# Performance work log

Measured on AMD Instinct MI355X. Metric: run time of the kernel, lower is better.

Reference implementation:

```python
import jax, jax.numpy as jnp
import numpy as np

K = 4                 # max_block_size (depthwise conv kernel size)
BLOCKS = (1, 2, 3, 4) # block sizes, offset 0
DS = 4                # downsample_factor
BLOCK_MULT = 12       # lcm(1,2,3,4)
DIM = 512
NUM_TOKENS = 256


def setup_inputs() -> dict:
    key = jax.random.key(0)
    ks = jax.random.split(key, 8)
    b, n = 4, 4096
    s = 0.02
    return {
        "x": jax.random.randint(ks[0], (b, n), 0, NUM_TOKENS),
        "emb": jax.random.normal(ks[1], (NUM_TOKENS, DIM), dtype=jnp.float32) * s,
        "conv_w": jax.random.normal(ks[2], (DIM, K), dtype=jnp.float32) * s,   # depthwise Conv1d weight [d,1,K] squeezed
        "conv_b": jax.random.normal(ks[3], (DIM,), dtype=jnp.float32) * s,
        "proj_w": jax.random.normal(ks[4], (DIM, DIM), dtype=jnp.float32) * s,  # 1x1 conv == linear [out,in]
        "proj_b": jax.random.normal(ks[5], (DIM,), dtype=jnp.float32) * s,
        "score_w": jax.random.normal(ks[6], (DIM,), dtype=jnp.float32) * s,     # nn.Linear(dim,1)
        "score_b": jax.random.normal(ks[7], (), dtype=jnp.float32) * s,
    }


def reference(x, emb, conv_w, conv_b, proj_w, proj_b, score_w, score_b):
    b, n = x.shape
    h = emb[x]  # [b, n, d] token embedding (gather)

    # pos_conv: pad (K-1) at sequence end, depthwise conv (valid), then pointwise proj
    hp = jnp.pad(h, ((0, 0), (0, K - 1), (0, 0)))
    y = conv_b + sum(hp[:, k:k + n, :] * conv_w[:, k] for k in range(K))  # [b, n, d]
    h = y @ proj_w.T + proj_b

    # pad sequence to multiple of lcm of block sizes
    L = -(-n // BLOCK_MULT) * BLOCK_MULT
    h = jnp.pad(h, ((0, 0), (0, L - n), (0, 0)))

    # multi-scale block mean pooling, upsampled back to length L
    reprs = []
    for bs in BLOCKS:
        r = h.reshape(b, L // bs, bs, DIM).mean(axis=2)     # [b, L/bs, d]
        reprs.append(jnp.repeat(r, bs, axis=1))             # [b, L, d]
    block_reprs = jnp.stack(reprs, axis=2)                  # [b, L, nb, d]

    # per-position block scores
    scores = block_reprs @ score_w + score_b                # [b, L, nb]
    scores = jax.nn.softmax(scores, axis=2)

    # consensus attention over positions (d = nb = len(BLOCKS))
    sim = jnp.einsum('bid,bjd->bij', scores, scores)        # [b, L, L]
    attn = jax.nn.softmax(sim, axis=-1)
    scores = jnp.einsum('bij,bjm->bim', attn, scores)       # [b, L, nb]

    # fuse block representations and downsample
    out = jnp.einsum('bnkd,bnk->bnd', block_reprs, scores)  # [b, L, d]
    m = -(-n // DS) * DS                                    # == n (4096 divisible by 4)
    out = out[:, :m].reshape(b, m // DS, DS, DIM).mean(axis=2)
    return out
```

## Files before the change

kernel.cpp:

```cpp
#include <hip/hip_runtime.h>
#include <hip/hip_bf16.h>

#define B_ 4
#define N_ 4096
#define L_ 4104
#define D_ 512
#define BK 64
#define NF 210
#define ZCH 36
#define ZCHUNKS 114
#define PST 37

typedef __attribute__((ext_vector_type(8))) short bf16x8;
typedef __attribute__((ext_vector_type(4))) float f32x4;

__global__ __launch_bounds__(256) void k_g(const float* __restrict__ emb,
    const float* __restrict__ pw, const float* __restrict__ cwp,
    const float* __restrict__ cb, const float* __restrict__ pb,
    float* __restrict__ G, float* __restrict__ biasp,
    unsigned* __restrict__ featPk, float* __restrict__ featCf,
    float* __restrict__ Zg) {
  __shared__ __align__(16) __hip_bfloat16 As[2][64 * BK];
  __shared__ __align__(16) __hip_bfloat16 Bs[2][128 * BK];
  __shared__ __align__(16) float cwS[512];
  __shared__ float red[4];
  const int bx = blockIdx.x;
  const int t = threadIdx.x;
  const int w = t >> 6, l = t & 63;

  if (bx == 128) {
    for (int zi = t; zi < B_ * NF * 5; zi += 256) Zg[zi] = 0.f;
    if (t < NF) {
      int idx = 0, mp = 0, mq = 0, mr = 0, ms = 0;
      for (int m = 0; m <= 6; ++m)
        for (int p = m; p >= 0; --p)
          for (int q = m - p; q >= 0; --q)
            for (int r = m - p - q; r >= 0; --r) {
              const int s4 = m - p - q - r;
              if (idx == t) { mp = p; mq = q; mr = r; ms = s4; }
              ++idx;
            }
      featPk[t] = (unsigned)mp | ((unsigned)mq << 8) | ((unsigned)mr << 16) | ((unsigned)ms << 24);
      const float invf[7] = {1.f, 1.f, 0.5f, 1.f/6.f, 1.f/24.f, 1.f/120.f, 1.f/720.f};
      featCf[t] = invf[mp] * invf[mq] * invf[mr] * invf[ms];
    }
    return;
  }
  if (bx >= 64) {
    const int o0 = (bx - 64) * 8;
    const float2 cv = *(const float2*)(cb + t * 2);
#pragma unroll
    for (int oo = 0; oo < 8; ++oo) {
      const int o = o0 + oo;
      const float2 wv = *(const float2*)(pw + (size_t)o * 512 + t * 2);
      float s = wv.x * cv.x + wv.y * cv.y;
#pragma unroll
      for (int off = 32; off > 0; off >>= 1) s += __shfl_xor(s, off);
      if (l == 0) red[w] = s;
      __syncthreads();
      if (t == 0) biasp[o] = red[0] + red[1] + red[2] + red[3] + pb[o];
      __syncthreads();
    }
    return;
  }

  const int m0 = (bx & 3) * 64;
  const int n0 = ((bx >> 2) & 3) * 128;
  const int kp = bx >> 4;
  const int quad = l >> 4, r16 = l & 15;
  const int wc = w * 32;

  cwS[t]       = cwp[t * 4 + kp];
  cwS[t + 256] = cwp[(t + 256) * 4 + kp];

  f32x4 acc[4][2];
#pragma unroll
  for (int a = 0; a < 4; ++a)
#pragma unroll
    for (int bq = 0; bq < 2; ++bq) acc[a][bq] = (f32x4){0.f, 0.f, 0.f, 0.f};

  const int ra = t >> 2, ga0 = (t & 3) * 2;
  const int rb = t >> 1, gb0 = (t & 1) * 4;

#define STAGEG(buf, kb)                                                          \
  _Pragma("unroll")                                                              \
  for (int gi = 0; gi < 2; ++gi) {                                               \
    const int g = ga0 + gi;                                                      \
    const int c0 = (kb) + g * 8;                                                 \
    const float4 a0 = *(const float4*)(emb + (size_t)(m0 + ra) * 512 + c0);      \
    const float4 a1 = *(const float4*)(emb + (size_t)(m0 + ra) * 512 + c0 + 4);  \
    const float4 w0 = *(const float4*)(cwS + c0);                                \
    const float4 w1 = *(const float4*)(cwS + c0 + 4);                            \
    union { __hip_bfloat16 q[8]; bf16x8 v; } ua;                                 \
    ua.q[0] = __float2bfloat16(a0.x * w0.x); ua.q[1] = __float2bfloat16(a0.y * w0.y); \
    ua.q[2] = __float2bfloat16(a0.z * w0.z); ua.q[3] = __float2bfloat16(a0.w * w0.w); \
    ua.q[4] = __float2bfloat16(a1.x * w1.x); ua.q[5] = __float2bfloat16(a1.y * w1.y); \
    ua.q[6] = __float2bfloat16(a1.z * w1.z); ua.q[7] = __float2bfloat16(a1.w * w1.w); \
    *(bf16x8*)(&As[buf][ra * BK + ((g ^ (ra & 7)) * 8)]) = ua.v;                 \
  }                                                                              \
  _Pragma("unroll")                                                              \
  for (int gi = 0; gi < 4; ++gi) {                                               \
    const int g = gb0 + gi;                                                      \
    const int c0 = (kb) + g * 8;                                                 \
    const float4 b0 = *(const float4*)(pw + (size_t)(n0 + rb) * 512 + c0);       \
    const float4 b1 = *(const float4*)(pw + (size_t)(n0 + rb) * 512 + c0 + 4);   \
    union { __hip_bfloat16 q[8]; bf16x8 v; } ub;                                 \
    ub.q[0] = __float2bfloat16(b0.x); ub.q[1] = __float2bfloat16(b0.y);          \
    ub.q[2] = __float2bfloat16(b0.z); ub.q[3] = __float2bfloat16(b0.w);          \
    ub.q[4] = __float2bfloat16(b1.x); ub.q[5] = __float2bfloat16(b1.y);          \
    ub.q[6] = __float2bfloat16(b1.z); ub.q[7] = __float2bfloat16(b1.w);          \
    *(bf16x8*)(&Bs[buf][rb * BK + ((g ^ (rb & 7)) * 8)]) = ub.v;                 \
  }

  __syncthreads();
  STAGEG(0, 0)
  __syncthreads();

#pragma unroll 1
  for (int kt = 0; kt < 8; ++kt) {
    const int cur = kt & 1;
    if (kt < 7) { STAGEG(1 - cur, (kt + 1) * BK) }
#pragma unroll
    for (int kk = 0; kk < 2; ++kk) {
      const int col_e = (kk * 32 + quad * 8) ^ ((r16 & 7) * 8);
      bf16x8 af[4], bfr[2];
#pragma unroll
      for (int ti = 0; ti < 4; ++ti)
        af[ti] = *(const bf16x8*)(&As[cur][(ti * 16 + r16) * BK + col_e]);
#pragma unroll
      for (int tj = 0; tj < 2; ++tj)
        bfr[tj] = *(const bf16x8*)(&Bs[cur][(wc + tj * 16 + r16) * BK + col_e]);
#pragma unroll
      for (int ti = 0; ti < 4; ++ti)
#pragma unroll
        for (int tj = 0; tj < 2; ++tj)
          acc[ti][tj] = __builtin_amdgcn_mfma_f32_16x16x32_bf16(af[ti], bfr[tj], acc[ti][tj], 0, 0, 0);
    }
    __syncthreads();
  }
#undef STAGEG

#pragma unroll
  for (int ti = 0; ti < 4; ++ti) {
    const int gi0 = m0 + ti * 16 + quad * 4;
#pragma unroll
    for (int tj = 0; tj < 2; ++tj) {
      const int go = n0 + wc + tj * 16 + r16;
#pragma unroll
      for (int r = 0; r < 4; ++r)
        G[((size_t)kp * 256 + gi0 + r) * 512 + go] = acc[ti][tj][r];
    }
  }
}

__global__ __launch_bounds__(256) void k_ts(const float* __restrict__ G,
    const float* __restrict__ biasp, const float* __restrict__ sw,
    float* __restrict__ TS, float* __restrict__ c0g) {
  __shared__ float red[4];
  const int bx = blockIdx.x;
  const int t = threadIdx.x, w = t >> 6, l = t & 63;
  if (bx == 128) {
    const float2 a = *(const float2*)(biasp + t * 2);
    const float2 b = *(const float2*)(sw + t * 2);
    float s = a.x * b.x + a.y * b.y;
#pragma unroll
    for (int off = 32; off > 0; off >>= 1) s += __shfl_xor(s, off);
    if (l == 0) red[w] = s;
    __syncthreads();
    if (t == 0) c0g[0] = red[0] + red[1] + red[2] + red[3];
    return;
  }
  const float4 s0 = *(const float4*)(sw + l * 8);
  const float4 s1 = *(const float4*)(sw + l * 8 + 4);
#pragma unroll
  for (int rr = 0; rr < 2; ++rr) {
    const int row = bx * 8 + w * 2 + rr;
    const float4 g0 = *(const float4*)(G + (size_t)row * 512 + l * 8);
    const float4 g1 = *(const float4*)(G + (size_t)row * 512 + l * 8 + 4);
    float s = g0.x * s0.x + g0.y * s0.y + g0.z * s0.z + g0.w * s0.w
            + g1.x * s1.x + g1.y * s1.y + g1.z * s1.z + g1.w * s1.w;
#pragma unroll
    for (int off = 32; off > 0; off >>= 1) s += __shfl_xor(s, off);
    if (l == 0) TS[row] = s;
  }
}

__device__ __forceinline__ float4 softmax4(const float* __restrict__ tw, int base,
                                           int i, float bb) {
  const float s0 = tw[i - base] + bb;
  const int j2 = i & ~1;
  const float s1 = (tw[j2 - base] + tw[j2 + 1 - base]) * 0.5f + bb;
  const int j3 = (i / 3) * 3;
  const float s2 = (tw[j3 - base] + tw[j3 + 1 - base] + tw[j3 + 2 - base]) * (1.f / 3.f) + bb;
  const int j4 = i & ~3;
  const float s3 = (tw[j4 - base] + tw[j4 + 1 - base] + tw[j4 + 2 - base] + tw[j4 + 3 - base]) * 0.25f + bb;
  const float m = fmaxf(fmaxf(s0, s1), fmaxf(s2, s3));
  const float e0 = __expf(s0 - m), e1 = __expf(s1 - m), e2 = __expf(s2 - m), e3 = __expf(s3 - m);
  const float inv = 1.f / (e0 + e1 + e2 + e3);
  return make_float4(e0 * inv, e1 * inv, e2 * inv, e3 * inv);
}

__global__ __launch_bounds__(256) void k_zphi(const int* __restrict__ x,
    const float* __restrict__ TS, const float* __restrict__ c0g,
    const float* __restrict__ sb, const unsigned* __restrict__ featPk,
    float* __restrict__ Zg) {
  __shared__ float twj[ZCH];
  __shared__ float P[32][PST];
  __shared__ unsigned pkS[NF];
  __shared__ int tokS[ZCH + 3];
  const int bx = blockIdx.x;
  const int b = bx / ZCHUNKS, jc = bx % ZCHUNKS;
  const int t = threadIdx.x;
  const int j0 = jc * ZCH;
  if (t < NF) pkS[t] = featPk[t];
  if (t < ZCH + 3) {
    const int j = j0 + t;
    tokS[t] = (j < N_) ? x[b * N_ + j] : -1;
  }
  __syncthreads();
  if (t < ZCH) {
    float tv = 0.f;
    if (j0 + t < N_) {
      tv = c0g[0];
#pragma unroll
      for (int k = 0; k < 4; ++k) {
        const int tk = tokS[t + k];
        if (tk >= 0) tv += TS[k * 256 + tk];
      }
    }
    twj[t] = tv;
  }
  __syncthreads();
  const float bb = sb[0];
  if (t < ZCH) {
    const float4 s = softmax4(twj, j0, j0 + t, bb);
    P[0][t] = 1.f; P[8][t] = 1.f; P[16][t] = 1.f; P[24][t] = 1.f;
    float va = 1.f, vb = 1.f, vc = 1.f, vd = 1.f;
#pragma unroll
    for (int e = 1; e < 8; ++e) {
      va *= s.x; vb *= s.y; vc *= s.z; vd *= s.w;
      P[e][t] = va; P[8 + e][t] = vb; P[16 + e][t] = vc; P[24 + e][t] = vd;
    }
  }
  __syncthreads();
  if (t < NF) {
    const unsigned pk = pkS[t];
    const int p = pk & 255, q = (pk >> 8) & 255, r = (pk >> 16) & 255, s4 = pk >> 24;
    const float* Ra0 = &P[p][0];       const float* Ra1 = &P[p + 1][0];
    const float* Rb0 = &P[8 + q][0];   const float* Rb1 = &P[8 + q + 1][0];
    const float* Rc0 = &P[16 + r][0];  const float* Rc1 = &P[16 + r + 1][0];
    const float* Rd0 = &P[24 + s4][0]; const float* Rd1 = &P[24 + s4 + 1][0];
    float z0 = 0.f, z1 = 0.f, z2 = 0.f, z3 = 0.f, z4 = 0.f;
#pragma unroll 4
    for (int jj = 0; jj < ZCH; ++jj) {
      const float pa0 = Ra0[jj], pa1 = Ra1[jj];
      const float pb0 = Rb0[jj], pb1 = Rb1[jj];
      const float pc0 = Rc0[jj], pc1 = Rc1[jj];
      const float pd0 = Rd0[jj], pd1 = Rd1[jj];
      const float cd = pc0 * pd0, ab = pa0 * pb0;
      z4 += pa0 * (pb0 * cd);
      z0 += pa1 * (pb0 * cd);
      z1 += pb1 * (pa0 * cd);
      z2 += pc1 * (ab * pd0);
      z3 += pd1 * (ab * pc0);
    }
    float* zb = Zg + (size_t)(b * NF + t) * 5;
    atomicAdd(zb + 0, z0); atomicAdd(zb + 1, z1); atomicAdd(zb + 2, z2);
    atomicAdd(zb + 3, z3); atomicAdd(zb + 4, z4);
  }
}

__global__ __launch_bounds__(256) void k_fuse(const int* __restrict__ x,
    const float* __restrict__ G, const float* __restrict__ biasp,
    const float* __restrict__ TS, const float* __restrict__ c0g,
    const float* __restrict__ sb, const unsigned* __restrict__ featPk,
    const float* __restrict__ featCf, const float* __restrict__ Zg,
    float* __restrict__ out) {
  __shared__ __align__(16) float4 wgtS[12];
  __shared__ float tbS[12];
  __shared__ float Pr[12][33];
  __shared__ float Zl[NF * 5];
  __shared__ unsigned pkS[NF];
  __shared__ float cfS[NF];
  __shared__ int tokS[16];
  const int bx = blockIdx.x;
  const int b = bx / 342, j12 = bx % 342;
  const int t = threadIdx.x, d = t * 2;
  const int r0 = 12 * j12;

  if (t < NF) { pkS[t] = featPk[t]; cfS[t] = featCf[t]; }
  for (int i2 = t; i2 < NF * 5; i2 += 256) Zl[i2] = Zg[(size_t)b * NF * 5 + i2];
  if (t < 15) {
    const int j = r0 + t;
    tokS[t] = (j < N_) ? x[b * N_ + j] : -1;
  }
  __syncthreads();

  const float2 bp = *(const float2*)(biasp + d);
  float2 hv[12];
#pragma unroll
  for (int q = 0; q < 12; ++q) {
    float2 a = make_float2(0.f, 0.f);
    if (r0 + q < N_) {
      a = bp;
#pragma unroll
      for (int k = 0; k < 4; ++k) {
        const int tk = tokS[q + k];
        if (tk >= 0) {
          const float2 g = *(const float2*)(G + ((size_t)k * 256 + tk) * 512 + d);
          a.x += g.x; a.y += g.y;
        }
      }
    }
    hv[q] = a;
  }

  if (t < 12) {
    float tv = 0.f;
    if (r0 + t < N_) {
      tv = c0g[0];
#pragma unroll
      for (int k = 0; k < 4; ++k) {
        const int tk = tokS[t + k];
        if (tk >= 0) tv += TS[k * 256 + tk];
      }
    }
    tbS[t] = tv;
  }
  __syncthreads();
  if (t < 12) {
    const float4 s = softmax4(tbS, r0, r0 + t, sb[0]);
    float* p = &Pr[t][0];
    float va = 1.f, vb = 1.f, vc = 1.f, vd = 1.f;
    p[0] = 1.f; p[8] = 1.f; p[16] = 1.f; p[24] = 1.f;
#pragma unroll
    for (int e = 1; e < 8; ++e) {
      va *= s.x; vb *= s.y; vc *= s.z; vd *= s.w;
      p[e] = va; p[8 + e] = vb; p[16 + e] = vc; p[24 + e] = vd;
    }
  }
  __syncthreads();
  if (t < 192) {
    const int row = t >> 4, fi = t & 15;
    float n0 = 0.f, n1 = 0.f, n2 = 0.f, n3 = 0.f, dn = 0.f;
    const float* pr = &Pr[row][0];
    for (int f = fi; f < NF; f += 16) {
      const unsigned pk = pkS[f];
      const float val = cfS[f] * pr[pk & 255] * pr[8 + ((pk >> 8) & 255)]
                                * pr[16 + ((pk >> 16) & 255)] * pr[24 + (pk >> 24)];
      const float* z = &Zl[f * 5];
      n0 += val * z[0]; n1 += val * z[1]; n2 += val * z[2]; n3 += val * z[3];
      dn += val * z[4];
    }
#pragma unroll
    for (int m = 8; m >= 1; m >>= 1) {
      n0 += __shfl_xor(n0, m); n1 += __shfl_xor(n1, m); n2 += __shfl_xor(n2, m);
      n3 += __shfl_xor(n3, m); dn += __shfl_xor(dn, m);
    }
    if (fi == 0) {
      const float inv = 1.f / dn;
      wgtS[row] = make_float4(n0 * inv, n1 * inv, n2 * inv, n3 * inv);
    }
  }
  __syncthreads();

  float2 p2[6], p3[4], p4[3];
#pragma unroll
  for (int g = 0; g < 6; ++g) {
    p2[g].x = (hv[2 * g].x + hv[2 * g + 1].x) * 0.5f;
    p2[g].y = (hv[2 * g].y + hv[2 * g + 1].y) * 0.5f;
  }
#pragma unroll
  for (int g = 0; g < 4; ++g) {
    p3[g].x = (hv[3 * g].x + hv[3 * g + 1].x + hv[3 * g + 2].x) * (1.f / 3.f);
    p3[g].y = (hv[3 * g].y + hv[3 * g + 1].y + hv[3 * g + 2].y) * (1.f / 3.f);
  }
#pragma unroll
  for (int g = 0; g < 3; ++g) {
    p4[g].x = (hv[4 * g].x + hv[4 * g + 1].x + hv[4 * g + 2].x + hv[4 * g + 3].x) * 0.25f;
    p4[g].y = (hv[4 * g].y + hv[4 * g + 1].y + hv[4 * g + 2].y + hv[4 * g + 3].y) * 0.25f;
  }

#pragma unroll
  for (int o = 0; o < 3; ++o) {
    const int orow = j12 * 3 + o;
    if (orow < 1024) {
      float ox = 0.f, oy = 0.f;
#pragma unroll
      for (int rr = 0; rr < 4; ++rr) {
        const int r = 4 * o + rr;
        const float4 wv = wgtS[r];
        const float2 p1 = hv[r];
        const float2 q2 = p2[r >> 1];
        const float2 q3 = p3[r / 3];
        const float2 q4 = p4[o];
        ox += wv.x * p1.x + wv.y * q2.x + wv.z * q3.x + wv.w * q4.x;
        oy += wv.x * p1.y + wv.y * q2.y + wv.z * q3.y + wv.w * q4.y;
      }
      float2 ov; ov.x = ox * 0.25f; ov.y = oy * 0.25f;
      *(float2*)(out + (size_t)(b * 1024 + orow) * D_ + d) = ov;
    }
  }
}

extern "C" void kernel_launch(void* const* d_in, const int* in_sizes, int n_in,
                              void* d_out, int out_size, void* d_ws, size_t ws_size,
                              hipStream_t stream) {
  const int*   x       = (const int*)d_in[0];
  const float* emb     = (const float*)d_in[1];
  const float* conv_w  = (const float*)d_in[2];
  const float* conv_b  = (const float*)d_in[3];
  const float* proj_w  = (const float*)d_in[4];
  const float* proj_b  = (const float*)d_in[5];
  const float* score_w = (const float*)d_in[6];
  const float* score_b = (const float*)d_in[7];
  float* out = (float*)d_out;

  char* ws = (char*)d_ws;
  size_t off = 0;
  float*    G      = (float*)(ws + off); off += (size_t)4 * 256 * 512 * 4;
  float*    bias   = (float*)(ws + off); off += (size_t)512 * 4;
  float*    Zg     = (float*)(ws + off); off += (size_t)B_ * NF * 5 * 4;
  unsigned* featPk = (unsigned*)(ws + off); off += (size_t)1024;
  float*    featCf = (float*)(ws + off); off += (size_t)1024;
  float*    TS     = (float*)(ws + off); off += (size_t)1024 * 4;
  float*    c0     = (float*)(ws + off); off += (size_t)16;
  (void)in_sizes; (void)n_in; (void)out_size; (void)ws_size;

  k_g<<<129, 256, 0, stream>>>(emb, proj_w, conv_w, conv_b, proj_b, G, bias, featPk, featCf, Zg);
  k_ts<<<129, 256, 0, stream>>>(G, bias, score_w, TS, c0);
  k_zphi<<<B_ * ZCHUNKS, 256, 0, stream>>>(x, TS, c0, score_b, featPk, Zg);
  k_fuse<<<B_ * 342, 256, 0, stream>>>(x, G, bias, TS, c0, score_b, featPk, featCf, Zg, out);
}
```

Before: 137.1 us.

## Merge four kernels into one cooperative persistent kernel with grid syncs

Replaces the four separate launches (GEMM, score projection, Z accumulation, fuse) with one cooperative kernel of 512 blocks. Phases are separated by grid.sync, and shared memory is overlaid through a union. The fuse phase now loops over tiles in grid-stride fashion. This removes launch gaps and inter-kernel drain costs, at the price of grid-wide barriers, a fixed grid size and lower per-phase parallelism in the fuse stage.

```diff
diff --git a/kernel.cpp b/kernel.cpp
--- a/kernel.cpp
+++ b/kernel.cpp
@@ -1,5 +1,8 @@
 #include <hip/hip_runtime.h>
 #include <hip/hip_bf16.h>
+#include <hip/hip_cooperative_groups.h>
+
+namespace cg = cooperative_groups;
 
 #define B_ 4
 #define N_ 4096
@@ -10,77 +13,68 @@
 #define ZCH 36
 #define ZCHUNKS 114
 #define PST 37
+#define GRID 512
 
 typedef __attribute__((ext_vector_type(8))) short bf16x8;
 typedef __attribute__((ext_vector_type(4))) float f32x4;
 
-__global__ __launch_bounds__(256) void k_g(const float* __restrict__ emb,
-    const float* __restrict__ pw, const float* __restrict__ cwp,
-    const float* __restrict__ cb, const float* __restrict__ pb,
+struct GS { __hip_bfloat16 As[2][64 * BK]; __hip_bfloat16 Bs[2][128 * BK]; float cwS[512]; };
+struct ZS { float twj[ZCH]; float P[32][PST]; unsigned pkS[NF]; int tokS[ZCH + 3]; };
+struct FS { float wgtS[48]; float tbS[12]; float Pr[12][33]; float Zl[NF * 5];
+            unsigned pkS[NF]; float cfS[NF]; int tokS[16]; };
+
+__device__ __forceinline__ float4 softmax4(const float* __restrict__ tw, int base,
+                                           int i, float bb) {
+  const float s0 = tw[i - base] + bb;
+  const int j2 = i & ~1;
+  const float s1 = (tw[j2 - base] + tw[j2 + 1 - base]) * 0.5f + bb;
+  const int j3 = (i / 3) * 3;
+  const float s2 = (tw[j3 - base] + tw[j3 + 1 - base] + tw[j3 + 2 - base]) * (1.f / 3.f) + bb;
+  const int j4 = i & ~3;
+  const float s3 = (tw[j4 - base] + tw[j4 + 1 - base] + tw[j4 + 2 - base] + tw[j4 + 3 - base]) * 0.25f + bb;
+  const float m = fmaxf(fmaxf(s0, s1), fmaxf(s2, s3));
+  const float e0 = __expf(s0 - m), e1 = __expf(s1 - m), e2 = __expf(s2 - m), e3 = __expf(s3 - m);
+  const float inv = 1.f / (e0 + e1 + e2 + e3);
+  return make_float4(e0 * inv, e1 * inv, e2 * inv, e3 * inv);
+}
+
+__global__ __launch_bounds__(256, 2) void k_all(const int* __restrict__ x,
+    const float* __restrict__ emb, const float* __restrict__ cwp,
+    const float* __restrict__ cb, const float* __restrict__ pw,
+    const float* __restrict__ pb, const float* __restrict__ sw,
+    const float* __restrict__ sb,
     float* __restrict__ G, float* __restrict__ biasp,
     unsigned* __restrict__ featPk, float* __restrict__ featCf,
-    float* __restrict__ Zg) {
-  __shared__ __align__(16) __hip_bfloat16 As[2][64 * BK];
-  __shared__ __align__(16) __hip_bfloat16 Bs[2][128 * BK];
-  __shared__ __align__(16) float cwS[512];
+    float* __restrict__ Zg, float* __restrict__ TS, float* __restrict__ c0g,
+    float* __restrict__ out) {
+  __shared__ __align__(16) union { GS g; ZS z; FS f; } u;
   __shared__ float red[4];
+  cg::grid_group grid = cg::this_grid();
   const int bx = blockIdx.x;
   const int t = threadIdx.x;
-  const int w = t >> 6, l = t & 63;
-
-  if (bx == 128) {
-    for (int zi = t; zi < B_ * NF * 5; zi += 256) Zg[zi] = 0.f;
-    if (t < NF) {
-      int idx = 0, mp = 0, mq = 0, mr = 0, ms = 0;
-      for (int m = 0; m <= 6; ++m)
-        for (int p = m; p >= 0; --p)
-          for (int q = m - p; q >= 0; --q)
-            for (int r = m - p - q; r >= 0; --r) {
-              const int s4 = m - p - q - r;
-              if (idx == t) { mp = p; mq = q; mr = r; ms = s4; }
-              ++idx;
-            }
-      featPk[t] = (unsigned)mp | ((unsigned)mq << 8) | ((unsigned)mr << 16) | ((unsigned)ms << 24);
-      const float invf[7] = {1.f, 1.f, 0.5f, 1.f/6.f, 1.f/24.f, 1.f/120.f, 1.f/720.f};
-      featCf[t] = invf[mp] * invf[mq] * invf[mr] * invf[ms];
-    }
-    return;
-  }
-  if (bx >= 64) {
-    const int o0 = (bx - 64) * 8;
-    const float2 cv = *(const float2*)(cb + t * 2);
-#pragma unroll
-    for (int oo = 0; oo < 8; ++oo) {
-      const int o = o0 + oo;
-      const float2 wv = *(const float2*)(pw + (size_t)o * 512 + t * 2);
-      float s = wv.x * cv.x + wv.y * cv.y;
-#pragma unroll
-      for (int off = 32; off > 0; off >>= 1) s += __shfl_xor(s, off);
-      if (l == 0) red[w] = s;
-      __syncthreads();
-      if (t == 0) biasp[o] = red[0] + red[1] + red[2] + red[3] + pb[o];
-      __syncthreads();
-    }
-    return;
-  }
-
-  const int m0 = (bx & 3) * 64;
-  const int n0 = ((bx >> 2) & 3) * 128;
-  const int kp = bx >> 4;
-  const int quad = l >> 4, r16 = l & 15;
-  const int wc = w * 32;
-
-  cwS[t]       = cwp[t * 4 + kp];
-  cwS[t + 256] = cwp[(t + 256) * 4 + kp];
-
-  f32x4 acc[4][2];
-#pragma unroll
-  for (int a = 0; a < 4; ++a)
-#pragma unroll
-    for (int bq = 0; bq < 2; ++bq) acc[a][bq] = (f32x4){0.f, 0.f, 0.f, 0.f};
-
-  const int ra = t >> 2, ga0 = (t & 3) * 2;
-  const int rb = t >> 1, gb0 = (t & 1) * 4;
+
+  if (bx < 64) {
+    const int w = t >> 6, l = t & 63;
+    const int m0 = (bx & 3) * 64;
+    const int n0 = ((bx >> 2) & 3) * 128;
+    const int kp = bx >> 4;
+    const int quad = l >> 4, r16 = l & 15;
+    const int wc = w * 32;
+    auto& As = u.g.As;
+    auto& Bs = u.g.Bs;
+    float* cwS = u.g.cwS;
+
+    cwS[t]       = cwp[t * 4 + kp];
+    cwS[t + 256] = cwp[(t + 256) * 4 + kp];
+
+    f32x4 acc[4][2];
+#pragma unroll
+    for (int a = 0; a < 4; ++a)
+#pragma unroll
+      for (int bq = 0; bq < 2; ++bq) acc[a][bq] = (f32x4){0.f, 0.f, 0.f, 0.f};
+
+    const int ra = t >> 2, ga0 = (t & 3) * 2;
+    const int rb = t >> 1, gb0 = (t & 1) * 4;
 
 #define STAGEG(buf, kb)                                                          \
   _Pragma("unroll")                                                              \
@@ -112,69 +106,85 @@
     *(bf16x8*)(&Bs[buf][rb * BK + ((g ^ (rb & 7)) * 8)]) = ub.v;                 \
   }
 
-  __syncthreads();
-  STAGEG(0, 0)
-  __syncthreads();
+    __syncthreads();
+    STAGEG(0, 0)
+    __syncthreads();
 
 #pragma unroll 1
-  for (int kt = 0; kt < 8; ++kt) {
-    const int cur = kt & 1;
-    if (kt < 7) { STAGEG(1 - cur, (kt + 1) * BK) }
-#pragma unroll
-    for (int kk = 0; kk < 2; ++kk) {
-      const int col_e = (kk * 32 + quad * 8) ^ ((r16 & 7) * 8);
-      bf16x8 af[4], bfr[2];
-#pragma unroll
-      for (int ti = 0; ti < 4; ++ti)
-        af[ti] = *(const bf16x8*)(&As[cur][(ti * 16 + r16) * BK + col_e]);
-#pragma unroll
-      for (int tj = 0; tj < 2; ++tj)
-        bfr[tj] = *(const bf16x8*)(&Bs[cur][(wc + tj * 16 + r16) * BK + col_e]);
-#pragma unroll
-      for (int ti = 0; ti < 4; ++ti)
+    for (int kt = 0; kt < 8; ++kt) {
+      const int cur = kt & 1;
+      if (kt < 7) { STAGEG(1 - cur, (kt + 1) * BK) }
+#pragma unroll
+      for (int kk = 0; kk < 2; ++kk) {
+        const int col_e = (kk * 32 + quad * 8) ^ ((r16 & 7) * 8);
+        bf16x8 af[4], bfr[2];
+#pragma unroll
+        for (int ti = 0; ti < 4; ++ti)
+          af[ti] = *(const bf16x8*)(&As[cur][(ti * 16 + r16) * BK + col_e]);
 #pragma unroll
         for (int tj = 0; tj < 2; ++tj)
-          acc[ti][tj] = __builtin_amdgcn_mfma_f32_16x16x32_bf16(af[ti], bfr[tj], acc[ti][tj], 0, 0, 0);
-    }
-    __syncthreads();
+          bfr[tj] = *(const bf16x8*)(&Bs[cur][(wc + tj * 16 + r16) * BK + col_e]);
+#pragma unroll
+        for (int ti = 0; ti < 4; ++ti)
+#pragma unroll
+          for (int tj = 0; tj < 2; ++tj)
+            acc[ti][tj] = __builtin_amdgcn_mfma_f32_16x16x32_bf16(af[ti], bfr[tj], acc[ti][tj], 0, 0, 0);
+      }
+      __syncthreads();
+    }
+#undef STAGEG
+
+#pragma unroll
+    for (int ti = 0; ti < 4; ++ti) {
+      const int gi0 = m0 + ti * 16 + quad * 4;
+#pragma unroll
+      for (int tj = 0; tj < 2; ++tj) {
+        const int go = n0 + wc + tj * 16 + r16;
+#pragma unroll
+        for (int r = 0; r < 4; ++r)
+          G[((size_t)kp * 256 + gi0 + r) * 512 + go] = acc[ti][tj][r];
+      }
+    }
+  } else if (bx < 96) {
+    const int w = t >> 6, l = t & 63;
+    const float4 cb0 = *(const float4*)(cb + l * 8);
+    const float4 cb1 = *(const float4*)(cb + l * 8 + 4);
+#pragma unroll
+    for (int i = 0; i < 4; ++i) {
+      const int o = (bx - 64) * 16 + w * 4 + i;
+      const float4 w0 = *(const float4*)(pw + (size_t)o * 512 + l * 8);
+      const float4 w1 = *(const float4*)(pw + (size_t)o * 512 + l * 8 + 4);
+      float s = w0.x * cb0.x + w0.y * cb0.y + w0.z * cb0.z + w0.w * cb0.w
+              + w1.x * cb1.x + w1.y * cb1.y + w1.z * cb1.z + w1.w * cb1.w;
+#pragma unroll
+      for (int off = 32; off > 0; off >>= 1) s += __shfl_xor(s, off);
+      if (l == 0) biasp[o] = s + pb[o];
+    }
+  } else if (bx == 96) {
+    for (int zi = t; zi < B_ * NF * 5; zi += 256) Zg[zi] = 0.f;
+    if (t < NF) {
+      int idx = 0, mp = 0, mq = 0, mr = 0, ms = 0;
+      for (int m = 0; m <= 6; ++m)
+        for (int p = m; p >= 0; --p)
+          for (int q = m - p; q >= 0; --q)
+            for (int r = m - p - q; r >= 0; --r) {
+              const int s4 = m - p - q - r;
+              if (idx == t) { mp = p; mq = q; mr = r; ms = s4; }
+              ++idx;
+            }
+      featPk[t] = (unsigned)mp | ((unsigned)mq << 8) | ((unsigned)mr << 16) | ((unsigned)ms << 24);
+      const float invf[7] = {1.f, 1.f, 0.5f, 1.f/6.f, 1.f/24.f, 1.f/120.f, 1.f/720.f};
+      featCf[t] = invf[mp] * invf[mq] * invf[mr] * invf[ms];
+    }
   }
-#undef STAGEG
-
-#pragma unroll
-  for (int ti = 0; ti < 4; ++ti) {
-    const int gi0 = m0 + ti * 16 + quad * 4;
-#pragma unroll
-    for (int tj = 0; tj < 2; ++tj) {
-      const int go = n0 + wc + tj * 16 + r16;
-#pragma unroll
-      for (int r = 0; r < 4; ++r)
-        G[((size_t)kp * 256 + gi0 + r) * 512 + go] = acc[ti][tj][r];
-    }
-  }
-}
-
-__global__ __launch_bounds__(256) void k_ts(const float* __restrict__ G,
-    const float* __restrict__ biasp, const float* __restrict__ sw,
-    float* __restrict__ TS, float* __restrict__ c0g) {
-  __shared__ float red[4];
-  const int bx = blockIdx.x;
-  const int t = threadIdx.x, w = t >> 6, l = t & 63;
-  if (bx == 128) {
-    const float2 a = *(const float2*)(biasp + t * 2);
-    const float2 b = *(const float2*)(sw + t * 2);
-    float s = a.x * b.x + a.y * b.y;
-#pragma unroll
-    for (int off = 32; off > 0; off >>= 1) s += __shfl_xor(s, off);
-    if (l == 0) red[w] = s;
-    __syncthreads();
-    if (t == 0) c0g[0] = red[0] + red[1] + red[2] + red[3];
-    return;
-  }
-  const float4 s0 = *(const float4*)(sw + l * 8);
-  const float4 s1 = *(const float4*)(sw + l * 8 + 4);
-#pragma unroll
-  for (int rr = 0; rr < 2; ++rr) {
-    const int row = bx * 8 + w * 2 + rr;
+
+  grid.sync();
+
+  if (bx < 256) {
+    const int w = t >> 6, l = t & 63;
+    const int row = bx * 4 + w;
+    const float4 s0 = *(const float4*)(sw + l * 8);
+    const float4 s1 = *(const float4*)(sw + l * 8 + 4);
     const float4 g0 = *(const float4*)(G + (size_t)row * 512 + l * 8);
     const float4 g1 = *(const float4*)(G + (size_t)row * 512 + l * 8 + 4);
     float s = g0.x * s0.x + g0.y * s0.y + g0.z * s0.z + g0.w * s0.w
@@ -182,223 +192,208 @@
 #pragma unroll
     for (int off = 32; off > 0; off >>= 1) s += __shfl_xor(s, off);
     if (l == 0) TS[row] = s;
+  } else if (bx == 256) {
+    const int w = t >> 6, l = t & 63;
+    const float2 a = *(const float2*)(biasp + t * 2);
+    const float2 b = *(const float2*)(sw + t * 2);
+    float s = a.x * b.x + a.y * b.y;
+#pragma unroll
+    for (int off = 32; off > 0; off >>= 1) s += __shfl_xor(s, off);
+    if (l == 0) red[w] = s;
+    __syncthreads();
+    if (t == 0) c0g[0] = red[0] + red[1] + red[2] + red[3];
   }
-}
-
-__device__ __forceinline__ float4 softmax4(const float* __restrict__ tw, int base,
-                                           int i, float bb) {
-  const float s0 = tw[i - base] + bb;
-  const int j2 = i & ~1;
-  const float s1 = (tw[j2 - base] + tw[j2 + 1 - base]) * 0.5f + bb;
-  const int j3 = (i / 3) * 3;
-  const float s2 = (tw[j3 - base] + tw[j3 + 1 - base] + tw[j3 + 2 - base]) * (1.f / 3.f) + bb;
-  const int j4 = i & ~3;
-  const float s3 = (tw[j4 - base] + tw[j4 + 1 - base] + tw[j4 + 2 - base] + tw[j4 + 3 - base]) * 0.25f + bb;
-  const float m = fmaxf(fmaxf(s0, s1), fmaxf(s2, s3));
-  const float e0 = __expf(s0 - m), e1 = __expf(s1 - m), e2 = __expf(s2 - m), e3 = __expf(s3 - m);
-  const float inv = 1.f / (e0 + e1 + e2 + e3);
-  return make_float4(e0 * inv, e1 * inv, e2 * inv, e3 * inv);
-}
-
-__global__ __launch_bounds__(256) void k_zphi(const int* __restrict__ x,
-    const float* __restrict__ TS, const float* __restrict__ c0g,
-    const float* __restrict__ sb, const unsigned* __restrict__ featPk,
-    float* __restrict__ Zg) {
-  __shared__ float twj[ZCH];
-  __shared__ float P[32][PST];
-  __shared__ unsigned pkS[NF];
-  __shared__ int tokS[ZCH + 3];
-  const int bx = blockIdx.x;
-  const int b = bx / ZCHUNKS, jc = bx % ZCHUNKS;
-  const int t = threadIdx.x;
-  const int j0 = jc * ZCH;
-  if (t < NF) pkS[t] = featPk[t];
-  if (t < ZCH + 3) {
-    const int j = j0 + t;
-    tokS[t] = (j < N_) ? x[b * N_ + j] : -1;
+
+  grid.sync();
+
+  if (bx < B_ * ZCHUNKS) {
+    const int b = bx / ZCHUNKS, jc = bx % ZCHUNKS;
+    const int j0 = jc * ZCH;
+    float* twj = u.z.twj;
+    float (&P)[32][PST] = u.z.P;
+    unsigned* pkS = u.z.pkS;
+    int* tokS = u.z.tokS;
+    if (t < NF) pkS[t] = featPk[t];
+    if (t < ZCH + 3) {
+      const int j = j0 + t;
+      tokS[t] = (j < N_) ? x[b * N_ + j] : -1;
+    }
+    __syncthreads();
+    if (t < ZCH) {
+      float tv = 0.f;
+      if (j0 + t < N_) {
+        tv = c0g[0];
+#pragma unroll
+        for (int k = 0; k < 4; ++k) {
+          const int tk = tokS[t + k];
+          if (tk >= 0) tv += TS[k * 256 + tk];
+        }
+      }
+      twj[t] = tv;
+    }
+    __syncthreads();
+    const float bb = sb[0];
+    if (t < ZCH) {
+      const float4 s = softmax4(twj, j0, j0 + t, bb);
+      P[0][t] = 1.f; P[8][t] = 1.f; P[16][t] = 1.f; P[24][t] = 1.f;
+      float va = 1.f, vb = 1.f, vc = 1.f, vd = 1.f;
+#pragma unroll
+      for (int e = 1; e < 8; ++e) {
+        va *= s.x; vb *= s.y; vc *= s.z; vd *= s.w;
+        P[e][t] = va; P[8 + e][t] = vb; P[16 + e][t] = vc; P[24 + e][t] = vd;
+      }
+    }
+    __syncthreads();
+    if (t < NF) {
+      const unsigned pk = pkS[t];
+      const int p = pk & 255, q = (pk >> 8) & 255, r = (pk >> 16) & 255, s4 = pk >> 24;
+      const float* Ra0 = &P[p][0];       const float* Ra1 = &P[p + 1][0];
+      const float* Rb0 = &P[8 + q][0];   const float* Rb1 = &P[8 + q + 1][0];
+      const float* Rc0 = &P[16 + r][0];  const float* Rc1 = &P[16 + r + 1][0];
+      const float* Rd0 = &P[24 + s4][0]; const float* Rd1 = &P[24 + s4 + 1][0];
+      float z0 = 0.f, z1 = 0.f, z2 = 0.f, z3 = 0.f, z4 = 0.f;
+#pragma unroll 4
+      for (int jj = 0; jj < ZCH; ++jj) {
+        const float pa0 = Ra0[jj], pa1 = Ra1[jj];
+        const float pb0 = Rb0[jj], pb1 = Rb1[jj];
+        const float pc0 = Rc0[jj], pc1 = Rc1[jj];
+        const float pd0 = Rd0[jj], pd1 = Rd1[jj];
+        const float cd = pc0 * pd0, ab = pa0 * pb0;
+        z4 += pa0 * (pb0 * cd);
+        z0 += pa1 * (pb0 * cd);
+        z1 += pb1 * (pa0 * cd);
+        z2 += pc1 * (ab * pd0);
+        z3 += pd1 * (ab * pc0);
+      }
+      float* zb = Zg + (size_t)(b * NF + t) * 5;
+      atomicAdd(zb + 0, z0); atomicAdd(zb + 1, z1); atomicAdd(zb + 2, z2);
+      atomicAdd(zb + 3, z3); atomicAdd(zb + 4, z4);
+    }
   }
-  __syncthreads();
-  if (t < ZCH) {
-    float tv = 0.f;
-    if (j0 + t < N_) {
-      tv = c0g[0];
-#pragma unroll
-      for (int k = 0; k < 4; ++k) {
-        const int tk = tokS[t + k];
-        if (tk >= 0) tv += TS[k * 256 + tk];
-      }
-    }
-    twj[t] = tv;
-  }
-  __syncthreads();
-  const float bb = sb[0];
-  if (t < ZCH) {
-    const float4 s = softmax4(twj, j0, j0 + t, bb);
-    P[0][t] = 1.f; P[8][t] = 1.f; P[16][t] = 1.f; P[24][t] = 1.f;
-    float va = 1.f, vb = 1.f, vc = 1.f, vd = 1.f;
-#pragma unroll
-    for (int e = 1; e < 8; ++e) {
-      va *= s.x; vb *= s.y; vc *= s.z; vd *= s.w;
-      P[e][t] = va; P[8 + e][t] = vb; P[16 + e][t] = vc; P[24 + e][t] = vd;
-    }
-  }
-  __syncthreads();
-  if (t < NF) {
-    const unsigned pk = pkS[t];
-    const int p = pk & 255, q = (pk >> 8) & 255, r = (pk >> 16) & 255, s4 = pk >> 24;
-    const float* Ra0 = &P[p][0];       const float* Ra1 = &P[p + 1][0];
-    const float* Rb0 = &P[8 + q][0];   const float* Rb1 = &P[8 + q + 1][0];
-    const float* Rc0 = &P[16 + r][0];  const float* Rc1 = &P[16 + r + 1][0];
-    const float* Rd0 = &P[24 + s4][0]; const float* Rd1 = &P[24 + s4 + 1][0];
-    float z0 = 0.f, z1 = 0.f, z2 = 0.f, z3 = 0.f, z4 = 0.f;
-#pragma unroll 4
-    for (int jj = 0; jj < ZCH; ++jj) {
-      const float pa0 = Ra0[jj], pa1 = Ra1[jj];
-      const float pb0 = Rb0[jj], pb1 = Rb1[jj];
-      const float pc0 = Rc0[jj], pc1 = Rc1[jj];
-      const float pd0 = Rd0[jj], pd1 = Rd1[jj];
-      const float cd = pc0 * pd0, ab = pa0 * pb0;
-      z4 += pa0 * (pb0 * cd);
-      z0 += pa1 * (pb0 * cd);
-      z1 += pb1 * (pa0 * cd);
-      z2 += pc1 * (ab * pd0);
-      z3 += pd1 * (ab * pc0);
-    }
-    float* zb = Zg + (size_t)(b * NF + t) * 5;
-    atomicAdd(zb + 0, z0); atomicAdd(zb + 1, z1); atomicAdd(zb + 2, z2);
-    atomicAdd(zb + 3, z3); atomicAdd(zb + 4, z4);
-  }
-}
-
-__global__ __launch_bounds__(256) void k_fuse(const int* __restrict__ x,
-    const float* __restrict__ G, const float* __restrict__ biasp,
-    const float* __restrict__ TS, const float* __restrict__ c0g,
-    const float* __restrict__ sb, const unsigned* __restrict__ featPk,
-    const float* __restrict__ featCf, const float* __restrict__ Zg,
-    float* __restrict__ out) {
-  __shared__ __align__(16) float4 wgtS[12];
-  __shared__ float tbS[12];
-  __shared__ float Pr[12][33];
-  __shared__ float Zl[NF * 5];
-  __shared__ unsigned pkS[NF];
-  __shared__ float cfS[NF];
-  __shared__ int tokS[16];
-  const int bx = blockIdx.x;
-  const int b = bx / 342, j12 = bx % 342;
-  const int t = threadIdx.x, d = t * 2;
-  const int r0 = 12 * j12;
-
-  if (t < NF) { pkS[t] = featPk[t]; cfS[t] = featCf[t]; }
-  for (int i2 = t; i2 < NF * 5; i2 += 256) Zl[i2] = Zg[(size_t)b * NF * 5 + i2];
-  if (t < 15) {
-    const int j = r0 + t;
-    tokS[t] = (j < N_) ? x[b * N_ + j] : -1;
-  }
-  __syncthreads();
-
-  const float2 bp = *(const float2*)(biasp + d);
-  float2 hv[12];
-#pragma unroll
-  for (int q = 0; q < 12; ++q) {
-    float2 a = make_float2(0.f, 0.f);
-    if (r0 + q < N_) {
-      a = bp;
-#pragma unroll
-      for (int k = 0; k < 4; ++k) {
-        const int tk = tokS[q + k];
-        if (tk >= 0) {
-          const float2 g = *(const float2*)(G + ((size_t)k * 256 + tk) * 512 + d);
-          a.x += g.x; a.y += g.y;
-        }
-      }
-    }
-    hv[q] = a;
-  }
-
-  if (t < 12) {
-    float tv = 0.f;
-    if (r0 + t < N_) {
-      tv = c0g[0];
-#pragma unroll
-      for (int k = 0; k < 4; ++k) {
-        const int tk = tokS[t + k];
-        if (tk >= 0) tv += TS[k * 256 + tk];
-      }
-    }
-    tbS[t] = tv;
-  }
-  __syncthreads();
-  if (t < 12) {
-    const float4 s = softmax4(tbS, r0, r0 + t, sb[0]);
-    float* p = &Pr[t][0];
-    float va = 1.f, vb = 1.f, vc = 1.f, vd = 1.f;
-    p[0] = 1.f; p[8] = 1.f; p[16] = 1.f; p[24] = 1.f;
-#pragma unroll
-    for (int e = 1; e < 8; ++e) {
-      va *= s.x; vb *= s.y; vc *= s.z; vd *= s.w;
-      p[e] = va; p[8 + e] = vb; p[16 + e] = vc; p[24 + e] = vd;
-    }
-  }
-  __syncthreads();
-  if (t < 192) {
-    const int row = t >> 4, fi = t & 15;
-    float n0 = 0.f, n1 = 0.f, n2 = 0.f, n3 = 0.f, dn = 0.f;
-    const float* pr = &Pr[row][0];
-    for (int f = fi; f < NF; f += 16) {
-      const unsigned pk = pkS[f];
-      const float val = cfS[f] * pr[pk & 255] * pr[8 + ((pk >> 8) & 255)]
-                                * pr[16 + ((pk >> 16) & 255)] * pr[24 + (pk >> 24)];
-      const float* z = &Zl[f * 5];
-      n0 += val * z[0]; n1 += val * z[1]; n2 += val * z[2]; n3 += val * z[3];
-      dn += val * z[4];
-    }
-#pragma unroll
-    for (int m = 8; m >= 1; m >>= 1) {
-      n0 += __shfl_xor(n0, m); n1 += __shfl_xor(n1, m); n2 += __shfl_xor(n2, m);
-      n3 += __shfl_xor(n3, m); dn += __shfl_xor(dn, m);
-    }
-    if (fi == 0) {
-      const float inv = 1.f / dn;
-      wgtS[row] = make_float4(n0 * inv, n1 * inv, n2 * inv, n3 * inv);
-    }
-  }
-  __syncthreads();
-
-  float2 p2[6], p3[4], p4[3];
-#pragma unroll
-  for (int g = 0; g < 6; ++g) {
-    p2[g].x = (hv[2 * g].x + hv[2 * g + 1].x) * 0.5f;
-    p2[g].y = (hv[2 * g].y + hv[2 * g + 1].y) * 0.5f;
-  }
-#pragma unroll
-  for (int g = 0; g < 4; ++g) {
-    p3[g].x = (hv[3 * g].x + hv[3 * g + 1].x + hv[3 * g + 2].x) * (1.f / 3.f);
-    p3[g].y = (hv[3 * g].y + hv[3 * g + 1].y + hv[3 * g + 2].y) * (1.f / 3.f);
-  }
-#pragma unroll
-  for (int g = 0; g < 3; ++g) {
-    p4[g].x = (hv[4 * g].x + hv[4 * g + 1].x + hv[4 * g + 2].x + hv[4 * g + 3].x) * 0.25f;
-    p4[g].y = (hv[4 * g].y + hv[4 * g + 1].y + hv[4 * g + 2].y + hv[4 * g + 3].y) * 0.25f;
-  }
-
-#pragma unroll
-  for (int o = 0; o < 3; ++o) {
-    const int orow = j12 * 3 + o;
-    if (orow < 1024) {
-      float ox = 0.f, oy = 0.f;
-#pragma unroll
-      for (int rr = 0; rr < 4; ++rr) {
-        const int r = 4 * o + rr;
-        const float4 wv = wgtS[r];
-        const float2 p1 = hv[r];
-        const float2 q2 = p2[r >> 1];
-        const float2 q3 = p3[r / 3];
-        const float2 q4 = p4[o];
-        ox += wv.x * p1.x + wv.y * q2.x + wv.z * q3.x + wv.w * q4.x;
-        oy += wv.x * p1.y + wv.y * q2.y + wv.z * q3.y + wv.w * q4.y;
-      }
-      float2 ov; ov.x = ox * 0.25f; ov.y = oy * 0.25f;
-      *(float2*)(out + (size_t)(b * 1024 + orow) * D_ + d) = ov;
+
+  grid.sync();
+
+  {
+    const int d = t * 2;
+    if (t < NF) { u.f.pkS[t] = featPk[t]; u.f.cfS[t] = featCf[t]; }
+    for (int tile = bx; tile < B_ * 342; tile += GRID) {
+      const int b = tile / 342, j12 = tile % 342;
+      const int r0 = 12 * j12;
+      for (int i2 = t; i2 < NF * 5; i2 += 256) u.f.Zl[i2] = Zg[(size_t)b * NF * 5 + i2];
+      if (t < 15) {
+        const int j = r0 + t;
+        u.f.tokS[t] = (j < N_) ? x[b * N_ + j] : -1;
+      }
+      __syncthreads();
+
+      const float2 bp = *(const float2*)(biasp + d);
+      float2 hv[12];
+#pragma unroll
+      for (int q = 0; q < 12; ++q) {
+        float2 a = make_float2(0.f, 0.f);
+        if (r0 + q < N_) {
+          a = bp;
+#pragma unroll
+          for (int k = 0; k < 4; ++k) {
+            const int tk = u.f.tokS[q + k];
+            if (tk >= 0) {
+              const float2 g = *(const float2*)(G + ((size_t)k * 256 + tk) * 512 + d);
+              a.x += g.x; a.y += g.y;
+            }
+          }
+        }
+        hv[q] = a;
+      }
+
+      if (t < 12) {
+        float tv = 0.f;
+        if (r0 + t < N_) {
+          tv = c0g[0];
+#pragma unroll
+          for (int k = 0; k < 4; ++k) {
+            const int tk = u.f.tokS[t + k];
+            if (tk >= 0) tv += TS[k * 256 + tk];
+          }
+        }
+        u.f.tbS[t] = tv;
+      }
+      __syncthreads();
+      if (t < 12) {
+        const float4 s = softmax4(u.f.tbS, r0, r0 + t, sb[0]);
+        float* p = &u.f.Pr[t][0];
+        float va = 1.f, vb = 1.f, vc = 1.f, vd = 1.f;
+        p[0] = 1.f; p[8] = 1.f; p[16] = 1.f; p[24] = 1.f;
+#pragma unroll
+        for (int e = 1; e < 8; ++e) {
+          va *= s.x; vb *= s.y; vc *= s.z; vd *= s.w;
+          p[e] = va; p[8 + e] = vb; p[16 + e] = vc; p[24 + e] = vd;
+        }
+      }
+      __syncthreads();
+      if (t < 192) {
+        const int row = t >> 4, fi = t & 15;
+        float n0 = 0.f, n1 = 0.f, n2 = 0.f, n3 = 0.f, dn = 0.f;
+        const float* pr = &u.f.Pr[row][0];
+        for (int f = fi; f < NF; f += 16) {
+          const unsigned pk = u.f.pkS[f];
+          const float val = u.f.cfS[f] * pr[pk & 255] * pr[8 + ((pk >> 8) & 255)]
+                                       * pr[16 + ((pk >> 16) & 255)] * pr[24 + (pk >> 24)];
+          const float* z = &u.f.Zl[f * 5];
+          n0 += val * z[0]; n1 += val * z[1]; n2 += val * z[2]; n3 += val * z[3];
+          dn += val * z[4];
+        }
+#pragma unroll
+        for (int m = 8; m >= 1; m >>= 1) {
+          n0 += __shfl_xor(n0, m); n1 += __shfl_xor(n1, m); n2 += __shfl_xor(n2, m);
+          n3 += __shfl_xor(n3, m); dn += __shfl_xor(dn, m);
+        }
+        if (fi == 0) {
+          const float inv = 1.f / dn;
+          u.f.wgtS[row * 4 + 0] = n0 * inv; u.f.wgtS[row * 4 + 1] = n1 * inv;
+          u.f.wgtS[row * 4 + 2] = n2 * inv; u.f.wgtS[row * 4 + 3] = n3 * inv;
+        }
+      }
+      __syncthreads();
+
+      float2 p2[6], p3[4], p4[3];
+#pragma unroll
+      for (int g = 0; g < 6; ++g) {
+        p2[g].x = (hv[2 * g].x + hv[2 * g + 1].x) * 0.5f;
+        p2[g].y = (hv[2 * g].y + hv[2 * g + 1].y) * 0.5f;
+      }
+#pragma unroll
+      for (int g = 0; g < 4; ++g) {
+        p3[g].x = (hv[3 * g].x + hv[3 * g + 1].x + hv[3 * g + 2].x) * (1.f / 3.f);
+        p3[g].y = (hv[3 * g].y + hv[3 * g + 1].y + hv[3 * g + 2].y) * (1.f / 3.f);
+      }
+#pragma unroll
+      for (int g = 0; g < 3; ++g) {
+        p4[g].x = (hv[4 * g].x + hv[4 * g + 1].x + hv[4 * g + 2].x + hv[4 * g + 3].x) * 0.25f;
+        p4[g].y = (hv[4 * g].y + hv[4 * g + 1].y + hv[4 * g + 2].y + hv[4 * g + 3].y) * 0.25f;
+      }
+
+#pragma unroll
+      for (int o = 0; o < 3; ++o) {
+        const int orow = j12 * 3 + o;
+        if (orow < 1024) {
+          float ox = 0.f, oy = 0.f;
+#pragma unroll
+          for (int rr = 0; rr < 4; ++rr) {
+            const int r = 4 * o + rr;
+            const float4 wv = make_float4(u.f.wgtS[r * 4], u.f.wgtS[r * 4 + 1],
+                                          u.f.wgtS[r * 4 + 2], u.f.wgtS[r * 4 + 3]);
+            const float2 p1 = hv[r];
+            const float2 q2 = p2[r >> 1];
+            const float2 q3 = p3[r / 3];
+            const float2 q4 = p4[o];
+            ox += wv.x * p1.x + wv.y * q2.x + wv.z * q3.x + wv.w * q4.x;
+            oy += wv.x * p1.y + wv.y * q2.y + wv.z * q3.y + wv.w * q4.y;
+          }
+          float2 ov; ov.x = ox * 0.25f; ov.y = oy * 0.25f;
+          *(float2*)(out + (size_t)(b * 1024 + orow) * D_ + d) = ov;
+        }
+      }
+      __syncthreads();
     }
   }
 }
@@ -427,8 +422,9 @@
   float*    c0     = (float*)(ws + off); off += (size_t)16;
   (void)in_sizes; (void)n_in; (void)out_size; (void)ws_size;
 
-  k_g<<<129, 256, 0, stream>>>(emb, proj_w, conv_w, conv_b, proj_b, G, bias, featPk, featCf, Zg);
-  k_ts<<<129, 256, 0, stream>>>(G, bias, score_w, TS, c0);
-  k_zphi<<<B_ * ZCHUNKS, 256, 0, stream>>>(x, TS, c0, score_b, featPk, Zg);
-  k_fuse<<<B_ * 342, 256, 0, stream>>>(x, G, bias, TS, c0, score_b, featPk, featCf, Zg, out);
+  void* args[] = { (void*)&x, (void*)&emb, (void*)&conv_w, (void*)&conv_b,
+                   (void*)&proj_w, (void*)&proj_b, (void*)&score_w, (void*)&score_b,
+                   (void*)&G, (void*)&bias, (void*)&featPk, (void*)&featCf,
+                   (void*)&Zg, (void*)&TS, (void*)&c0, (void*)&out };
+  hipLaunchCooperativeKernel((void*)k_all, dim3(GRID), dim3(256), args, 0, stream);
 }
```

Result: slower. 328.3 us (+139.4%).

## Compute token scores algebraically and merge score kernel into GEMM kernel

Applied to the files above, without the earlier changes.

Removes the separate k_ts kernel. Token scores are now computed inside k_g by dedicated blocks that form u = proj_wᵀ·score_w, scale it by each conv tap, and dot it with the embedding rows, so they no longer depend on G. The constant c0 is folded in the same way, and the bias blocks now do warp-level reductions without block syncs. This saves one kernel launch and the serial dependency on G, but runs an extra pass over proj_w in four blocks and uses fp32 rather than the bf16 GEMM path for the scores, which could change numerics slightly.

```diff
diff --git a/kernel.cpp b/kernel.cpp
--- a/kernel.cpp
+++ b/kernel.cpp
@@ -14,21 +14,77 @@
 typedef __attribute__((ext_vector_type(8))) short bf16x8;
 typedef __attribute__((ext_vector_type(4))) float f32x4;
 
+struct GemmS { __hip_bfloat16 As[2][64 * BK]; __hip_bfloat16 Bs[2][128 * BK]; float cwS[512]; };
+struct TsS   { float swS[512]; float uPart[4][512]; float vkS[512]; };
+
 __global__ __launch_bounds__(256) void k_g(const float* __restrict__ emb,
     const float* __restrict__ pw, const float* __restrict__ cwp,
     const float* __restrict__ cb, const float* __restrict__ pb,
+    const float* __restrict__ sw,
     float* __restrict__ G, float* __restrict__ biasp,
     unsigned* __restrict__ featPk, float* __restrict__ featCf,
-    float* __restrict__ Zg) {
-  __shared__ __align__(16) __hip_bfloat16 As[2][64 * BK];
-  __shared__ __align__(16) __hip_bfloat16 Bs[2][128 * BK];
-  __shared__ __align__(16) float cwS[512];
+    float* __restrict__ Zg, float* __restrict__ TS, float* __restrict__ c0g) {
+  __shared__ __align__(16) union { GemmS g; TsS ts; } u;
   __shared__ float red[4];
   const int bx = blockIdx.x;
   const int t = threadIdx.x;
   const int w = t >> 6, l = t & 63;
 
-  if (bx == 128) {
+  if (bx >= 97) {
+    const int kp = bx - 97;
+    float* swS = u.ts.swS;
+    float* vkS = u.ts.vkS;
+    swS[t] = sw[t]; swS[t + 256] = sw[t + 256];
+    __syncthreads();
+    const int c8 = l * 8;
+    float4 acc0 = {0.f, 0.f, 0.f, 0.f}, acc1 = {0.f, 0.f, 0.f, 0.f};
+    const int o0 = w * 128;
+#pragma unroll 4
+    for (int oo = 0; oo < 128; ++oo) {
+      const int o = o0 + oo;
+      const float so = swS[o];
+      const float4 w0 = *(const float4*)(pw + (size_t)o * 512 + c8);
+      const float4 w1 = *(const float4*)(pw + (size_t)o * 512 + c8 + 4);
+      acc0.x += so * w0.x; acc0.y += so * w0.y; acc0.z += so * w0.z; acc0.w += so * w0.w;
+      acc1.x += so * w1.x; acc1.y += so * w1.y; acc1.z += so * w1.z; acc1.w += so * w1.w;
+    }
+    *(float4*)(&u.ts.uPart[w][c8])     = acc0;
+    *(float4*)(&u.ts.uPart[w][c8 + 4]) = acc1;
+    __syncthreads();
+    const int c2 = t * 2;
+    const float uu0 = u.ts.uPart[0][c2] + u.ts.uPart[1][c2]
+                    + u.ts.uPart[2][c2] + u.ts.uPart[3][c2];
+    const float uu1 = u.ts.uPart[0][c2 + 1] + u.ts.uPart[1][c2 + 1]
+                    + u.ts.uPart[2][c2 + 1] + u.ts.uPart[3][c2 + 1];
+    vkS[c2]     = uu0 * cwp[c2 * 4 + kp];
+    vkS[c2 + 1] = uu1 * cwp[(c2 + 1) * 4 + kp];
+    if (kp == 0) {
+      float part = cb[c2] * uu0 + cb[c2 + 1] * uu1
+                 + pb[c2] * swS[c2] + pb[c2 + 1] * swS[c2 + 1];
+#pragma unroll
+      for (int m = 32; m >= 1; m >>= 1) part += __shfl_xor(part, m);
+      if (l == 0) red[w] = part;
+    }
+    __syncthreads();
+    if (kp == 0 && t == 0) c0g[0] = red[0] + red[1] + red[2] + red[3];
+    const int r16 = t & 15, tg = t >> 4;
+    for (int tok0 = 0; tok0 < 256; tok0 += 16) {
+      const int tok = tok0 + tg;
+      float dot = 0.f;
+#pragma unroll
+      for (int it = 0; it < 8; ++it) {
+        const int c = it * 64 + r16 * 4;
+        const float4 e4 = *(const float4*)(emb + (size_t)tok * 512 + c);
+        const float4 v4 = *(const float4*)(vkS + c);
+        dot += e4.x * v4.x + e4.y * v4.y + e4.z * v4.z + e4.w * v4.w;
+      }
+#pragma unroll
+      for (int m = 8; m >= 1; m >>= 1) dot += __shfl_xor(dot, m);
+      if (r16 == 0) TS[kp * 256 + tok] = dot;
+    }
+    return;
+  }
+  if (bx == 96) {
     for (int zi = t; zi < B_ * NF * 5; zi += 256) Zg[zi] = 0.f;
     if (t < NF) {
       int idx = 0, mp = 0, mq = 0, mr = 0, ms = 0;
@@ -47,19 +103,18 @@
     return;
   }
   if (bx >= 64) {
-    const int o0 = (bx - 64) * 8;
-    const float2 cv = *(const float2*)(cb + t * 2);
-#pragma unroll
-    for (int oo = 0; oo < 8; ++oo) {
-      const int o = o0 + oo;
-      const float2 wv = *(const float2*)(pw + (size_t)o * 512 + t * 2);
-      float s = wv.x * cv.x + wv.y * cv.y;
+    const float4 cb0 = *(const float4*)(cb + l * 8);
+    const float4 cb1 = *(const float4*)(cb + l * 8 + 4);
+#pragma unroll
+    for (int i = 0; i < 4; ++i) {
+      const int o = (bx - 64) * 16 + w * 4 + i;
+      const float4 w0 = *(const float4*)(pw + (size_t)o * 512 + l * 8);
+      const float4 w1 = *(const float4*)(pw + (size_t)o * 512 + l * 8 + 4);
+      float s = w0.x * cb0.x + w0.y * cb0.y + w0.z * cb0.z + w0.w * cb0.w
+              + w1.x * cb1.x + w1.y * cb1.y + w1.z * cb1.z + w1.w * cb1.w;
 #pragma unroll
       for (int off = 32; off > 0; off >>= 1) s += __shfl_xor(s, off);
-      if (l == 0) red[w] = s;
-      __syncthreads();
-      if (t == 0) biasp[o] = red[0] + red[1] + red[2] + red[3] + pb[o];
-      __syncthreads();
+      if (l == 0) biasp[o] = s + pb[o];
     }
     return;
   }
@@ -69,6 +124,9 @@
   const int kp = bx >> 4;
   const int quad = l >> 4, r16 = l & 15;
   const int wc = w * 32;
+  auto& As = u.g.As;
+  auto& Bs = u.g.Bs;
+  float* cwS = u.g.cwS;
 
   cwS[t]       = cwp[t * 4 + kp];
   cwS[t + 256] = cwp[(t + 256) * 4 + kp];
@@ -153,38 +211,6 @@
   }
 }
 
-__global__ __launch_bounds__(256) void k_ts(const float* __restrict__ G,
-    const float* __restrict__ biasp, const float* __restrict__ sw,
-    float* __restrict__ TS, float* __restrict__ c0g) {
-  __shared__ float red[4];
-  const int bx = blockIdx.x;
-  const int t = threadIdx.x, w = t >> 6, l = t & 63;
-  if (bx == 128) {
-    const float2 a = *(const float2*)(biasp + t * 2);
-    const float2 b = *(const float2*)(sw + t * 2);
-    float s = a.x * b.x + a.y * b.y;
-#pragma unroll
-    for (int off = 32; off > 0; off >>= 1) s += __shfl_xor(s, off);
-    if (l == 0) red[w] = s;
-    __syncthreads();
-    if (t == 0) c0g[0] = red[0] + red[1] + red[2] + red[3];
-    return;
-  }
-  const float4 s0 = *(const float4*)(sw + l * 8);
-  const float4 s1 = *(const float4*)(sw + l * 8 + 4);
-#pragma unroll
-  for (int rr = 0; rr < 2; ++rr) {
-    const int row = bx * 8 + w * 2 + rr;
-    const float4 g0 = *(const float4*)(G + (size_t)row * 512 + l * 8);
-    const float4 g1 = *(const float4*)(G + (size_t)row * 512 + l * 8 + 4);
-    float s = g0.x * s0.x + g0.y * s0.y + g0.z * s0.z + g0.w * s0.w
-            + g1.x * s1.x + g1.y * s1.y + g1.z * s1.z + g1.w * s1.w;
-#pragma unroll
-    for (int off = 32; off > 0; off >>= 1) s += __shfl_xor(s, off);
-    if (l == 0) TS[row] = s;
-  }
-}
-
 __device__ __forceinline__ float4 softmax4(const float* __restrict__ tw, int base,
                                            int i, float bb) {
   const float s0 = tw[i - base] + bb;
@@ -427,8 +453,8 @@
   float*    c0     = (float*)(ws + off); off += (size_t)16;
   (void)in_sizes; (void)n_in; (void)out_size; (void)ws_size;
 
-  k_g<<<129, 256, 0, stream>>>(emb, proj_w, conv_w, conv_b, proj_b, G, bias, featPk, featCf, Zg);
-  k_ts<<<129, 256, 0, stream>>>(G, bias, score_w, TS, c0);
+  k_g<<<101, 256, 0, stream>>>(emb, proj_w, conv_w, conv_b, proj_b, score_w,
+                               G, bias, featPk, featCf, Zg, TS, c0);
   k_zphi<<<B_ * ZCHUNKS, 256, 0, stream>>>(x, TS, c0, score_b, featPk, Zg);
   k_fuse<<<B_ * 342, 256, 0, stream>>>(x, G, bias, TS, c0, score_b, featPk, featCf, Zg, out);
 }
```

Result: slower. 141.0 us (+2.8%).
